# Performance work log

Measured on AMD Instinct MI355X. Metric: run time of the kernel, lower is better.

Reference implementation:

```python
import jax, jax.numpy as jnp
import numpy as np

DIM = 128
N_NODES = 100000
N_EDGES = 200000
M = 800000  # incidence pairs in each direction
L = 2
N_CLASS = 10


def setup_inputs() -> dict:
    key = jax.random.key(0)
    ks = jax.random.split(key, 8)
    s = 1.0 / np.sqrt(DIM)
    return {
        "node_x": jax.random.normal(ks[0], (N_NODES, DIM), jnp.float32),
        "nodes_map": jax.random.randint(ks[1], (M,), 0, N_NODES, jnp.int32),
        "edge_seg": jnp.sort(jax.random.randint(ks[2], (M,), 0, N_EDGES, jnp.int32)),
        "edges_map": jax.random.randint(ks[3], (M,), 0, N_EDGES, jnp.int32),
        "node_seg": jnp.sort(jax.random.randint(ks[4], (M,), 0, N_NODES, jnp.int32)),
        "num_edges": N_EDGES,
        "W_e": jax.random.normal(ks[5], (L, DIM, DIM), jnp.float32) * s,
        "b_e": jnp.zeros((L, DIM), jnp.float32),
        "g_e": jnp.ones((L, DIM), jnp.float32),
        "be_e": jnp.zeros((L, DIM), jnp.float32),
        "W_n": jax.random.normal(ks[6], (L, DIM, DIM), jnp.float32) * s,
        "b_n": jnp.zeros((L, DIM), jnp.float32),
        "g_n": jnp.ones((L, DIM), jnp.float32),
        "be_n": jnp.zeros((L, DIM), jnp.float32),
        "W_c": jax.random.normal(ks[7], (DIM, N_CLASS), jnp.float32) * s,
        "b_c": jnp.zeros((N_CLASS,), jnp.float32),
    }


def _seg_mean(x, seg, num_segments):
    # global_mean_pool: segment sum / count (count clamped to 1 for empty segments)
    s = jax.ops.segment_sum(x, seg, num_segments=num_segments)
    cnt = jax.ops.segment_sum(jnp.ones((x.shape[0],), x.dtype), seg, num_segments=num_segments)
    return s / jnp.maximum(cnt, 1.0)[:, None]


def _layernorm(x, g, b, eps=1e-5):
    m = jnp.mean(x, axis=-1, keepdims=True)
    v = jnp.mean(jnp.square(x - m), axis=-1, keepdims=True)
    return (x - m) * jax.lax.rsqrt(v + eps) * g + b


def reference(node_x, nodes_map, edge_seg, edges_map, node_seg, num_edges,
              W_e, b_e, g_e, be_e, W_n, b_n, g_n, be_n, W_c, b_c):
    n_nodes = node_x.shape[0]
    x = node_x  # in_drp = Dropout(0.0) is identity
    for i in range(W_e.shape[0]):
        # N2E: gather node feats per (edge, member) pair, mean-pool per hyperedge
        ex = _seg_mean(x[nodes_map], edge_seg, num_edges)          # [E, DIM]
        ex = jax.nn.relu(_layernorm(ex @ W_e[i] + b_e[i], g_e[i], be_e[i]))
        # E2N: gather edge feats per (node, incident-edge) pair, mean-pool per node
        x = _seg_mean(ex[edges_map], node_seg, n_nodes)            # [N, DIM]
        x = jax.nn.relu(_layernorm(x @ W_n[i] + b_n[i], g_n[i], be_n[i]))
    return jax.nn.log_softmax(x @ W_c + b_c, axis=-1)
```

## Files before the change

### kernel.cpp

```cpp
#include <hip/hip_runtime.h>
#include <hip/hip_bf16.h>

#define DIM 128

typedef __bf16 bf16x8 __attribute__((ext_vector_type(8)));
typedef float f32x4 __attribute__((ext_vector_type(4)));

static inline int cdiv(int a, int b) { return (a + b - 1) / b; }
static inline size_t align256(size_t x) { return (x + 255) & ~size_t(255); }

__device__ inline unsigned short f2bf(float f) {
    union { float f; unsigned int u; } v; v.f = f;
    unsigned int r = v.u + 0x7fff + ((v.u >> 16) & 1);
    return (unsigned short)(r >> 16);
}
__device__ inline unsigned int hb(float f) {
    return (__builtin_bit_cast(unsigned int, f) + 0x8000u) >> 16;
}

__global__ void seg_offsets_kernel(const int* __restrict__ seg, int m, int nseg,
                                   int* __restrict__ off) {
    int s = blockIdx.x * blockDim.x + threadIdx.x;
    if (s > nseg) return;
    int lo = 0, hi = m;
    while (lo < hi) {
        int mid = (lo + hi) >> 1;
        if (seg[mid] < s) lo = mid + 1; else hi = mid;
    }
    off[s] = lo;
}

__global__ void f32_to_bf16_kernel(const float* __restrict__ in,
                                   unsigned short* __restrict__ out, int n4) {
    int i = blockIdx.x * blockDim.x + threadIdx.x;
    if (i >= n4) return;
    float4 v = ((const float4*)in)[i];
    ushort4 o;
    o.x = f2bf(v.x); o.y = f2bf(v.y); o.z = f2bf(v.z); o.w = f2bf(v.w);
    ((ushort4*)out)[i] = o;
}

__global__ void swizzle_w_kernel(const float* __restrict__ W_e, const float* __restrict__ W_n,
                                 unsigned short* __restrict__ wsw) {
    int gid = blockIdx.x * blockDim.x + threadIdx.x;
    int mi = gid >> 11;
    int e = gid & 2047;
    const float* W = (mi < 2) ? (W_e + (size_t)mi * DIM * DIM)
                              : (W_n + (size_t)(mi - 2) * DIM * DIM);
    int t = e >> 9, n = (e >> 6) & 7, lane = e & 63;
    int q = lane >> 4, c = lane & 15;
    int k0 = t * 32 + q * 8, col = n * 16 + c;
    unsigned short vals[8];
#pragma unroll
    for (int j = 0; j < 8; ++j) vals[j] = f2bf(W[(size_t)(k0 + j) * DIM + col]);
    ushort4* dst = (ushort4*)(wsw + (size_t)gid * 8);
    dst[0] = make_ushort4(vals[0], vals[1], vals[2], vals[3]);
    dst[1] = make_ushort4(vals[4], vals[5], vals[6], vals[7]);
}

__device__ inline void accum8s(float* a, uint4 v, float wt) {
    unsigned int u[4] = {v.x, v.y, v.z, v.w};
#pragma unroll
    for (int i = 0; i < 4; ++i) {
        float lo = __builtin_bit_cast(float, u[i] << 16);
        float hi = __builtin_bit_cast(float, u[i]);
        a[2 * i]     = fmaf(wt, lo, a[2 * i]);
        a[2 * i + 1] = fmaf(wt, hi, a[2 * i + 1]);
    }
}

__global__ __launch_bounds__(512)
void fused_pool_gemm_ln_relu_v5_kernel(const uint4* __restrict__ src,
                                       const int* __restrict__ map,
                                       const int* __restrict__ off,
                                       const unsigned short* __restrict__ Wsw,
                                       const float* __restrict__ b,
                                       const float* __restrict__ g,
                                       const float* __restrict__ be,
                                       unsigned short* __restrict__ Y,
                                       int nseg) {
    __shared__ bf16x8 wlds[2048];
    __shared__ unsigned short alds[128 * 128];
    int tid = threadIdx.x;
    int w = tid >> 6, lane = tid & 63;
    int q = lane >> 4, c = lane & 15;

    {
        const uint4* gsrc = (const uint4*)Wsw;
        uint4* ldst = (uint4*)wlds;
#pragma unroll
        for (int i = 0; i < 4; ++i) ldst[tid + i * 512] = gsrc[tid + i * 512];
    }

    int blockbase = blockIdx.x * 128;
    int wavebase = w * 16;

    float bcol[8], gcol[8], becol[8];
#pragma unroll
    for (int n = 0; n < 8; ++n) {
        int col = n * 16 + c;
        bcol[n] = b[col]; gcol[n] = g[col]; becol[n] = be[col];
    }
    int begv[4], endv[4];
#pragma unroll
    for (int it = 0; it < 4; ++it) {
        int sc = min(blockbase + wavebase + it * 4 + q, nseg - 1);
        begv[it] = off[sc];
        endv[it] = off[sc + 1];
    }

    __syncthreads();

    const char* sbase = (const char*)src;
    unsigned cb = (unsigned)(c << 4);
    for (int it = 0; it < 4; ++it) {
        int s_local = wavebase + it * 4 + q;
        int beg = begv[it], end = endv[it];
        float a[8] = {0.f, 0.f, 0.f, 0.f, 0.f, 0.f, 0.f, 0.f};
        for (int j = beg; j < end; j += 4) {
            int j1 = min(j + 1, end - 1), j2 = min(j + 2, end - 1), j3 = min(j + 3, end - 1);
            unsigned r0 = (unsigned)map[j], r1 = (unsigned)map[j1];
            unsigned r2 = (unsigned)map[j2], r3 = (unsigned)map[j3];
            uint4 v0 = *(const uint4*)(sbase + ((r0 << 8) + cb));
            uint4 v1 = *(const uint4*)(sbase + ((r1 << 8) + cb));
            uint4 v2 = *(const uint4*)(sbase + ((r2 << 8) + cb));
            uint4 v3 = *(const uint4*)(sbase + ((r3 << 8) + cb));
            accum8s(a, v0, 1.f);
            accum8s(a, v1, (j + 1 < end) ? 1.f : 0.f);
            accum8s(a, v2, (j + 2 < end) ? 1.f : 0.f);
            accum8s(a, v3, (j + 3 < end) ? 1.f : 0.f);
        }
        float inv = 1.f / fmaxf((float)(end - beg), 1.f);
        uint4 o;
        o.x = hb(a[0] * inv) | (hb(a[1] * inv) << 16);
        o.y = hb(a[2] * inv) | (hb(a[3] * inv) << 16);
        o.z = hb(a[4] * inv) | (hb(a[5] * inv) << 16);
        o.w = hb(a[6] * inv) | (hb(a[7] * inv) << 16);
        uint4* wrow = (uint4*)(alds + (size_t)s_local * 128);
        wrow[c ^ (s_local & 7)] = o;
    }

    f32x4 acc[8];
#pragma unroll
    for (int n = 0; n < 8; ++n) acc[n] = f32x4{bcol[n], bcol[n], bcol[n], bcol[n]};

    const uint4* arow = (const uint4*)(alds + (size_t)(wavebase + c) * 128);
    int key = c & 7;
    bf16x8 a0 = *(const bf16x8*)&arow[(q + 0) ^ key];
    bf16x8 a1 = *(const bf16x8*)&arow[(q + 4) ^ key];
    bf16x8 a2 = *(const bf16x8*)&arow[(q + 8) ^ key];
    bf16x8 a3 = *(const bf16x8*)&arow[(q + 12) ^ key];

#pragma unroll
    for (int n = 0; n < 8; ++n) {
        acc[n] = __builtin_amdgcn_mfma_f32_16x16x32_bf16(a0, wlds[(0 * 8 + n) * 64 + lane], acc[n], 0, 0, 0);
        acc[n] = __builtin_amdgcn_mfma_f32_16x16x32_bf16(a1, wlds[(1 * 8 + n) * 64 + lane], acc[n], 0, 0, 0);
        acc[n] = __builtin_amdgcn_mfma_f32_16x16x32_bf16(a2, wlds[(2 * 8 + n) * 64 + lane], acc[n], 0, 0, 0);
        acc[n] = __builtin_amdgcn_mfma_f32_16x16x32_bf16(a3, wlds[(3 * 8 + n) * 64 + lane], acc[n], 0, 0, 0);
    }

    float s1[4], s2[4];
#pragma unroll
    for (int j = 0; j < 4; ++j) {
        float t1 = 0.f, t2 = 0.f;
#pragma unroll
        for (int n = 0; n < 8; ++n) { float v = acc[n][j]; t1 += v; t2 = fmaf(v, v, t2); }
        s1[j] = t1; s2[j] = t2;
    }
#pragma unroll
    for (int o = 1; o < 16; o <<= 1)
#pragma unroll
        for (int j = 0; j < 4; ++j) {
            s1[j] += __shfl_xor(s1[j], o);
            s2[j] += __shfl_xor(s2[j], o);
        }

#pragma unroll
    for (int j = 0; j < 4; ++j) {
        int row = blockbase + wavebase + q * 4 + j;
        if (row >= nseg) continue;
        float m = s1[j] * (1.f / DIM);
        float var = fmaf(-m, m, s2[j] * (1.f / DIM));
        float inv = rsqrtf(var + 1e-5f);
        unsigned short* yp = Y + (size_t)row * DIM + c;
#pragma unroll
        for (int n = 0; n < 8; ++n) {
            float d = acc[n][j] - m;
            float y = fmaxf(fmaf(d * inv, gcol[n], becol[n]), 0.f);
            unsigned int u = __builtin_bit_cast(unsigned int, y) + 0x8000u;
            yp[n * 16] = (unsigned short)(u >> 16);
        }
    }
}

#define CL_ROWS 4
__global__ __launch_bounds__(256)
void classifier_logsoftmax_v3_kernel(const uint4* __restrict__ X,
                                     const float* __restrict__ Wc,
                                     const float* __restrict__ bc,
                                     float* __restrict__ out, int nrows) {
    int w = threadIdx.x >> 6, lane = threadIdx.x & 63;
    int g = lane >> 4, c16 = lane & 15;
    int r0 = (blockIdx.x * 16 + w * 4 + g) * CL_ROWS;
    if (r0 >= nrows) return;

    float wc[8][10];
#pragma unroll
    for (int j = 0; j < 8; ++j)
#pragma unroll
        for (int c = 0; c < 10; ++c) wc[j][c] = Wc[(c16 * 8 + j) * 10 + c];
    float bcv[10];
#pragma unroll
    for (int c = 0; c < 10; ++c) bcv[c] = bc[c];

    int rend = min(r0 + CL_ROWS, nrows);
    for (int r = r0; r < rend; ++r) {
        uint4 v = X[(size_t)r * 16 + c16];
        float x[8];
        {
            unsigned int u[4] = {v.x, v.y, v.z, v.w};
#pragma unroll
            for (int i = 0; i < 4; ++i) {
                union { unsigned int ui; float f; } lo, hi;
                lo.ui = u[i] << 16;
                hi.ui = u[i] & 0xffff0000u;
                x[2 * i] = lo.f; x[2 * i + 1] = hi.f;
            }
        }
        float acc[10];
#pragma unroll
        for (int c = 0; c < 10; ++c) acc[c] = 0.f;
#pragma unroll
        for (int j = 0; j < 8; ++j)
#pragma unroll
            for (int c = 0; c < 10; ++c) acc[c] = fmaf(x[j], wc[j][c], acc[c]);

#pragma unroll
        for (int o = 1; o < 16; o <<= 1)
#pragma unroll
            for (int c = 0; c < 10; ++c) acc[c] += __shfl_xor(acc[c], o);

#pragma unroll
        for (int c = 0; c < 10; ++c) acc[c] += bcv[c];

        float mx = acc[0];
#pragma unroll
        for (int c = 1; c < 10; ++c) mx = fmaxf(mx, acc[c]);
        float se = 0.f;
#pragma unroll
        for (int c = 0; c < 10; ++c) se += expf(acc[c] - mx);
        float lse = mx + logf(se);

        float myv = 0.f;
#pragma unroll
        for (int c = 0; c < 10; ++c) myv = (c16 == c) ? acc[c] : myv;
        if (c16 < 10) out[(size_t)r * 10 + c16] = myv - lse;
    }
}

extern "C" void kernel_launch(void* const* d_in, const int* in_sizes, int n_in,
                              void* d_out, int out_size, void* d_ws, size_t ws_size,
                              hipStream_t stream) {
    const float* node_x    = (const float*)d_in[0];
    const int*   nodes_map = (const int*)d_in[1];
    const int*   edge_seg  = (const int*)d_in[2];
    const int*   edges_map = (const int*)d_in[3];
    const int*   node_seg  = (const int*)d_in[4];
    const float* W_e = (const float*)d_in[6];
    const float* b_e = (const float*)d_in[7];
    const float* g_e = (const float*)d_in[8];
    const float* be_e= (const float*)d_in[9];
    const float* W_n = (const float*)d_in[10];
    const float* b_n = (const float*)d_in[11];
    const float* g_n = (const float*)d_in[12];
    const float* be_n= (const float*)d_in[13];
    const float* W_c = (const float*)d_in[14];
    const float* b_c = (const float*)d_in[15];
    float* out = (float*)d_out;

    const int N = in_sizes[0] / DIM;
    const int M = in_sizes[1];
    const int E = 200000;
    const int L = in_sizes[6] / (DIM * DIM);

    char* ws = (char*)d_ws;
    int* edge_off = (int*)ws;           ws += align256((size_t)(E + 1) * sizeof(int));
    int* node_off = (int*)ws;           ws += align256((size_t)(N + 1) * sizeof(int));
    unsigned short* wsw = (unsigned short*)ws;      ws += align256((size_t)4 * 2048 * 8 * sizeof(unsigned short));
    unsigned short* node_xb = (unsigned short*)ws;  ws += align256((size_t)N * DIM * sizeof(unsigned short));
    unsigned short* exb = (unsigned short*)ws;      ws += align256((size_t)E * DIM * sizeof(unsigned short));
    unsigned short* xb  = (unsigned short*)ws;      ws += align256((size_t)N * DIM * sizeof(unsigned short));
    (void)ws_size;

    seg_offsets_kernel<<<cdiv(E + 1, 256), 256, 0, stream>>>(edge_seg, M, E, edge_off);
    seg_offsets_kernel<<<cdiv(N + 1, 256), 256, 0, stream>>>(node_seg, M, N, node_off);
    f32_to_bf16_kernel<<<cdiv(N * DIM / 4, 256), 256, 0, stream>>>(node_x, node_xb, N * DIM / 4);
    swizzle_w_kernel<<<32, 256, 0, stream>>>(W_e, W_n, wsw);

    const unsigned short* xcur = node_xb;
    for (int i = 0; i < L; ++i) {
        fused_pool_gemm_ln_relu_v5_kernel<<<cdiv(E, 128), 512, 0, stream>>>(
            (const uint4*)xcur, nodes_map, edge_off, wsw + (size_t)i * 16384,
            b_e + i * DIM, g_e + i * DIM, be_e + i * DIM, exb, E);
        fused_pool_gemm_ln_relu_v5_kernel<<<cdiv(N, 128), 512, 0, stream>>>(
            (const uint4*)exb, edges_map, node_off, wsw + (size_t)(2 + i) * 16384,
            b_n + i * DIM, g_n + i * DIM, be_n + i * DIM, xb, N);
        xcur = xb;
    }

    classifier_logsoftmax_v3_kernel<<<cdiv(N, 16 * CL_ROWS), 256, 0, stream>>>(
        (const uint4*)xcur, W_c, b_c, out, N);
}
```

Measured before the change: 349.4 us.

## Fuse classifier into final E2N kernel, merge offset kernels, prefetch map indices

Fuses the classifier and log-softmax into the epilogue of the last node-pooling kernel. The final node features stay in registers, rounded to bf16, and are multiplied by W_c with shuffle reductions, so the bf16 node tensor is never written and read back. Merges the two segment-offset binary-search launches into one. Software-prefetches the next four map indices in the gather loop to hide index-load latency. The trade-off is more register pressure in the classifier variant and W_c reloaded from global memory per thread.

Result: no change. 355.4 us (+1.7%).

```diff
diff --git a/kernel.cpp b/kernel.cpp
--- a/kernel.cpp
+++ b/kernel.cpp
@@ -18,16 +18,22 @@
     return (__builtin_bit_cast(unsigned int, f) + 0x8000u) >> 16;
 }
 
-__global__ void seg_offsets_kernel(const int* __restrict__ seg, int m, int nseg,
-                                   int* __restrict__ off) {
-    int s = blockIdx.x * blockDim.x + threadIdx.x;
-    if (s > nseg) return;
-    int lo = 0, hi = m;
-    while (lo < hi) {
-        int mid = (lo + hi) >> 1;
-        if (seg[mid] < s) lo = mid + 1; else hi = mid;
-    }
-    off[s] = lo;
+__global__ void seg_offsets2_kernel(const int* __restrict__ segA, int mA, int nA,
+                                    int* __restrict__ offA,
+                                    const int* __restrict__ segB, int mB, int nB,
+                                    int* __restrict__ offB) {
+    int i = blockIdx.x * blockDim.x + threadIdx.x;
+    if (i <= nA) {
+        int lo = 0, hi = mA;
+        while (lo < hi) { int mid = (lo + hi) >> 1; if (segA[mid] < i) lo = mid + 1; else hi = mid; }
+        offA[i] = lo;
+    }
+    int j = i - (nA + 1);
+    if (j >= 0 && j <= nB) {
+        int lo = 0, hi = mB;
+        while (lo < hi) { int mid = (lo + hi) >> 1; if (segB[mid] < j) lo = mid + 1; else hi = mid; }
+        offB[j] = lo;
+    }
 }
 
 __global__ void f32_to_bf16_kernel(const float* __restrict__ in,
@@ -69,8 +75,9 @@
     }
 }
 
+template <bool DO_CLS>
 __global__ __launch_bounds__(512)
-void fused_pool_gemm_ln_relu_v5_kernel(const uint4* __restrict__ src,
+void fused_pool_gemm_ln_relu_v6_kernel(const uint4* __restrict__ src,
                                        const int* __restrict__ map,
                                        const int* __restrict__ off,
                                        const unsigned short* __restrict__ Wsw,
@@ -78,6 +85,9 @@
                                        const float* __restrict__ g,
                                        const float* __restrict__ be,
                                        unsigned short* __restrict__ Y,
+                                       const float* __restrict__ Wc,
+                                       const float* __restrict__ bc,
+                                       float* __restrict__ cls_out,
                                        int nseg) {
     __shared__ bf16x8 wlds[2048];
     __shared__ unsigned short alds[128 * 128];
@@ -116,19 +126,27 @@
     for (int it = 0; it < 4; ++it) {
         int s_local = wavebase + it * 4 + q;
         int beg = begv[it], end = endv[it];
+        int e1 = max(end - 1, 0);
         float a[8] = {0.f, 0.f, 0.f, 0.f, 0.f, 0.f, 0.f, 0.f};
+        unsigned r0 = (unsigned)map[min(beg, e1)];
+        unsigned r1 = (unsigned)map[min(beg + 1, e1)];
+        unsigned r2 = (unsigned)map[min(beg + 2, e1)];
+        unsigned r3 = (unsigned)map[min(beg + 3, e1)];
         for (int j = beg; j < end; j += 4) {
-            int j1 = min(j + 1, end - 1), j2 = min(j + 2, end - 1), j3 = min(j + 3, end - 1);
-            unsigned r0 = (unsigned)map[j], r1 = (unsigned)map[j1];
-            unsigned r2 = (unsigned)map[j2], r3 = (unsigned)map[j3];
             uint4 v0 = *(const uint4*)(sbase + ((r0 << 8) + cb));
             uint4 v1 = *(const uint4*)(sbase + ((r1 << 8) + cb));
             uint4 v2 = *(const uint4*)(sbase + ((r2 << 8) + cb));
             uint4 v3 = *(const uint4*)(sbase + ((r3 << 8) + cb));
+            int jn = j + 4;
+            unsigned n0 = (unsigned)map[min(jn, e1)];
+            unsigned n1 = (unsigned)map[min(jn + 1, e1)];
+            unsigned n2 = (unsigned)map[min(jn + 2, e1)];
+            unsigned n3 = (unsigned)map[min(jn + 3, e1)];
             accum8s(a, v0, 1.f);
             accum8s(a, v1, (j + 1 < end) ? 1.f : 0.f);
             accum8s(a, v2, (j + 2 < end) ? 1.f : 0.f);
             accum8s(a, v3, (j + 3 < end) ? 1.f : 0.f);
+            r0 = n0; r1 = n1; r2 = n2; r3 = n3;
         }
         float inv = 1.f / fmaxf((float)(end - beg), 1.f);
         uint4 o;
@@ -178,83 +196,78 @@
 #pragma unroll
     for (int j = 0; j < 4; ++j) {
         int row = blockbase + wavebase + q * 4 + j;
-        if (row >= nseg) continue;
         float m = s1[j] * (1.f / DIM);
         float var = fmaf(-m, m, s2[j] * (1.f / DIM));
         float inv = rsqrtf(var + 1e-5f);
-        unsigned short* yp = Y + (size_t)row * DIM + c;
-#pragma unroll
-        for (int n = 0; n < 8; ++n) {
-            float d = acc[n][j] - m;
-            float y = fmaxf(fmaf(d * inv, gcol[n], becol[n]), 0.f);
-            unsigned int u = __builtin_bit_cast(unsigned int, y) + 0x8000u;
-            yp[n * 16] = (unsigned short)(u >> 16);
-        }
-    }
-}
-
-#define CL_ROWS 4
-__global__ __launch_bounds__(256)
-void classifier_logsoftmax_v3_kernel(const uint4* __restrict__ X,
-                                     const float* __restrict__ Wc,
-                                     const float* __restrict__ bc,
-                                     float* __restrict__ out, int nrows) {
-    int w = threadIdx.x >> 6, lane = threadIdx.x & 63;
-    int g = lane >> 4, c16 = lane & 15;
-    int r0 = (blockIdx.x * 16 + w * 4 + g) * CL_ROWS;
-    if (r0 >= nrows) return;
-
-    float wc[8][10];
-#pragma unroll
-    for (int j = 0; j < 8; ++j)
-#pragma unroll
-        for (int c = 0; c < 10; ++c) wc[j][c] = Wc[(c16 * 8 + j) * 10 + c];
-    float bcv[10];
-#pragma unroll
-    for (int c = 0; c < 10; ++c) bcv[c] = bc[c];
-
-    int rend = min(r0 + CL_ROWS, nrows);
-    for (int r = r0; r < rend; ++r) {
-        uint4 v = X[(size_t)r * 16 + c16];
-        float x[8];
-        {
-            unsigned int u[4] = {v.x, v.y, v.z, v.w};
-#pragma unroll
-            for (int i = 0; i < 4; ++i) {
-                union { unsigned int ui; float f; } lo, hi;
-                lo.ui = u[i] << 16;
-                hi.ui = u[i] & 0xffff0000u;
-                x[2 * i] = lo.f; x[2 * i + 1] = hi.f;
+        if (!DO_CLS) {
+            if (row >= nseg) continue;
+            unsigned short* yp = Y + (size_t)row * DIM + c;
+#pragma unroll
+            for (int n = 0; n < 8; ++n) {
+                float d = acc[n][j] - m;
+                float y = fmaxf(fmaf(d * inv, gcol[n], becol[n]), 0.f);
+                unsigned int u = __builtin_bit_cast(unsigned int, y) + 0x8000u;
+                yp[n * 16] = (unsigned short)(u >> 16);
             }
-        }
-        float acc[10];
-#pragma unroll
-        for (int c = 0; c < 10; ++c) acc[c] = 0.f;
-#pragma unroll
-        for (int j = 0; j < 8; ++j)
-#pragma unroll
-            for (int c = 0; c < 10; ++c) acc[c] = fmaf(x[j], wc[j][c], acc[c]);
-
-#pragma unroll
-        for (int o = 1; o < 16; o <<= 1)
-#pragma unroll
-            for (int c = 0; c < 10; ++c) acc[c] += __shfl_xor(acc[c], o);
-
-#pragma unroll
-        for (int c = 0; c < 10; ++c) acc[c] += bcv[c];
-
-        float mx = acc[0];
-#pragma unroll
-        for (int c = 1; c < 10; ++c) mx = fmaxf(mx, acc[c]);
-        float se = 0.f;
-#pragma unroll
-        for (int c = 0; c < 10; ++c) se += expf(acc[c] - mx);
-        float lse = mx + logf(se);
-
-        float myv = 0.f;
-#pragma unroll
-        for (int c = 0; c < 10; ++c) myv = (c16 == c) ? acc[c] : myv;
-        if (c16 < 10) out[(size_t)r * 10 + c16] = myv - lse;
+        } else {
+#pragma unroll
+            for (int n = 0; n < 8; ++n) {
+                float d = acc[n][j] - m;
+                float y = fmaxf(fmaf(d * inv, gcol[n], becol[n]), 0.f);
+                unsigned int u = (__builtin_bit_cast(unsigned int, y) + 0x8000u) & 0xffff0000u;
+                acc[n][j] = __builtin_bit_cast(float, u);
+            }
+        }
+    }
+
+    if (DO_CLS) {
+        float bcv[10];
+#pragma unroll
+        for (int t = 0; t < 10; ++t) bcv[t] = bc[t];
+#pragma unroll
+        for (int half = 0; half < 2; ++half) {
+            float ca[2][10];
+#pragma unroll
+            for (int jj = 0; jj < 2; ++jj)
+#pragma unroll
+                for (int t = 0; t < 10; ++t) ca[jj][t] = 0.f;
+#pragma unroll
+            for (int n = 0; n < 8; ++n) {
+                int col = n * 16 + c;
+                float wcn[10];
+#pragma unroll
+                for (int t = 0; t < 10; ++t) wcn[t] = Wc[col * 10 + t];
+                float x0 = acc[n][2 * half], x1 = acc[n][2 * half + 1];
+#pragma unroll
+                for (int t = 0; t < 10; ++t) {
+                    ca[0][t] = fmaf(x0, wcn[t], ca[0][t]);
+                    ca[1][t] = fmaf(x1, wcn[t], ca[1][t]);
+                }
+            }
+#pragma unroll
+            for (int o = 1; o < 16; o <<= 1)
+#pragma unroll
+                for (int jj = 0; jj < 2; ++jj)
+#pragma unroll
+                    for (int t = 0; t < 10; ++t) ca[jj][t] += __shfl_xor(ca[jj][t], o);
+#pragma unroll
+            for (int jj = 0; jj < 2; ++jj) {
+                int j = 2 * half + jj;
+                int row = blockbase + wavebase + q * 4 + j;
+                if (row >= nseg) continue;
+                float lv[10];
+#pragma unroll
+                for (int t = 0; t < 10; ++t) lv[t] = ca[jj][t] + bcv[t];
+                float mx = lv[0];
+#pragma unroll
+                for (int t = 1; t < 10; ++t) mx = fmaxf(mx, lv[t]);
+                float se = 0.f;
+#pragma unroll
+                for (int t = 0; t < 10; ++t) se += expf(lv[t] - mx);
+                float lse = mx + logf(se);
+                if (c < 10) cls_out[(size_t)row * 10 + c] = lv[c] - lse;
+            }
+        }
     }
 }
 
@@ -292,22 +305,28 @@
     unsigned short* xb  = (unsigned short*)ws;      ws += align256((size_t)N * DIM * sizeof(unsigned short));
     (void)ws_size;
 
-    seg_offsets_kernel<<<cdiv(E + 1, 256), 256, 0, stream>>>(edge_seg, M, E, edge_off);
-    seg_offsets_kernel<<<cdiv(N + 1, 256), 256, 0, stream>>>(node_seg, M, N, node_off);
+    seg_offsets2_kernel<<<cdiv(E + N + 2, 256), 256, 0, stream>>>(
+        edge_seg, M, E, edge_off, node_seg, M, N, node_off);
     f32_to_bf16_kernel<<<cdiv(N * DIM / 4, 256), 256, 0, stream>>>(node_x, node_xb, N * DIM / 4);
     swizzle_w_kernel<<<32, 256, 0, stream>>>(W_e, W_n, wsw);
 
     const unsigned short* xcur = node_xb;
     for (int i = 0; i < L; ++i) {
-        fused_pool_gemm_ln_relu_v5_kernel<<<cdiv(E, 128), 512, 0, stream>>>(
+        fused_pool_gemm_ln_relu_v6_kernel<false><<<cdiv(E, 128), 512, 0, stream>>>(
             (const uint4*)xcur, nodes_map, edge_off, wsw + (size_t)i * 16384,
-            b_e + i * DIM, g_e + i * DIM, be_e + i * DIM, exb, E);
-        fused_pool_gemm_ln_relu_v5_kernel<<<cdiv(N, 128), 512, 0, stream>>>(
-            (const uint4*)exb, edges_map, node_off, wsw + (size_t)(2 + i) * 16384,
-            b_n + i * DIM, g_n + i * DIM, be_n + i * DIM, xb, N);
-        xcur = xb;
-    }
-
-    classifier_logsoftmax_v3_kernel<<<cdiv(N, 16 * CL_ROWS), 256, 0, stream>>>(
-        (const uint4*)xcur, W_c, b_c, out, N);
-}
+            b_e + i * DIM, g_e + i * DIM, be_e + i * DIM, exb,
+            nullptr, nullptr, nullptr, E);
+        if (i < L - 1) {
+            fused_pool_gemm_ln_relu_v6_kernel<false><<<cdiv(N, 128), 512, 0, stream>>>(
+                (const uint4*)exb, edges_map, node_off, wsw + (size_t)(2 + i) * 16384,
+                b_n + i * DIM, g_n + i * DIM, be_n + i * DIM, xb,
+                nullptr, nullptr, nullptr, N);
+            xcur = xb;
+        } else {
+            fused_pool_gemm_ln_relu_v6_kernel<true><<<cdiv(N, 128), 512, 0, stream>>>(
+                (const uint4*)exb, edges_map, node_off, wsw + (size_t)(2 + i) * 16384,
+                b_n + i * DIM, g_n + i * DIM, be_n + i * DIM, nullptr,
+                W_c, b_c, out, N);
+        }
+    }
+}
```
